# Kernel optimization log

Measured on AMD Instinct MI355X. Metric: run time of the kernel, lower is better.

The kernel has to match this reference:

```python
import jax, jax.numpy as jnp
import numpy as np


def setup_inputs() -> dict:
    key = jax.random.key(0)
    k1, k2, k3, k4 = jax.random.split(key, 4)
    N, C, H, W = 4, 256, 64, 64
    Co, kh, kw, dg = 256, 3, 3, 1
    x = jax.random.normal(k1, (N, C, H, W), dtype=jnp.float32)
    offset = jax.random.normal(k2, (N, 2 * dg * kh * kw, H, W), dtype=jnp.float32)
    mask = jax.random.uniform(k3, (N, dg * kh * kw, H, W), dtype=jnp.float32)
    weight = jax.random.normal(k4, (Co, C, kh, kw), dtype=jnp.float32) * 0.02
    bias = jnp.zeros((Co,), dtype=jnp.float32)
    return {"x": x, "offset": offset, "mask": mask, "weight": weight, "bias": bias,
            "stride": 1, "padding": 1, "dilation": 1, "deformable_groups": 1}


def _dcn_v2(x, offset, mask, weight, bias, stride, padding, dilation, dg):
    N, C, H, W = x.shape
    Co, Ci, kh, kw = weight.shape
    K = kh * kw
    Ho, Wo = offset.shape[2], offset.shape[3]
    Cg = C // dg

    off = offset.reshape(N, dg, K, 2, Ho, Wo)
    dy, dx = off[:, :, :, 0], off[:, :, :, 1]          # [N,dg,K,Ho,Wo]
    m = mask.reshape(N, dg, K, Ho, Wo)

    ki = (jnp.arange(K) // kw).astype(jnp.float32)      # kernel row index
    kj = (jnp.arange(K) % kw).astype(jnp.float32)       # kernel col index
    base_y = (jnp.arange(Ho, dtype=jnp.float32) * stride - padding)
    base_x = (jnp.arange(Wo, dtype=jnp.float32) * stride - padding)
    # sampling coordinates [N,dg,K,Ho,Wo]
    py = dy + base_y[None, None, None, :, None] + (ki * dilation)[None, None, :, None, None]
    px = dx + base_x[None, None, None, None, :] + (kj * dilation)[None, None, :, None, None]

    y0 = jnp.floor(py)
    x0 = jnp.floor(px)
    wy1 = py - y0
    wx1 = px - x0
    wy0 = 1.0 - wy1
    wx0 = 1.0 - wx1
    y0i = y0.astype(jnp.int32)
    x0i = x0.astype(jnp.int32)

    xr = x.reshape(N, dg, Cg, H * W)

    def gather(yi, xi):
        valid = ((yi >= 0) & (yi < H) & (xi >= 0) & (xi < W)).astype(x.dtype)
        idx = jnp.clip(yi, 0, H - 1) * W + jnp.clip(xi, 0, W - 1)   # [N,dg,K,Ho,Wo]
        flat = idx.reshape(N, dg, 1, K * Ho * Wo)
        g = jnp.take_along_axis(xr, flat, axis=-1).reshape(N, dg, Cg, K, Ho, Wo)
        return g * valid[:, :, None]

    sampled = (gather(y0i, x0i) * (wy0 * wx0)[:, :, None]
               + gather(y0i, x0i + 1) * (wy0 * wx1)[:, :, None]
               + gather(y0i + 1, x0i) * (wy1 * wx0)[:, :, None]
               + gather(y0i + 1, x0i + 1) * (wy1 * wx1)[:, :, None])
    sampled = sampled * m[:, :, None]                     # modulation
    sampled = sampled.reshape(N, C, K, Ho, Wo)

    out = jnp.einsum('nckhw,ock->nohw', sampled, weight.reshape(Co, C, K))
    return out + bias[None, :, None, None]


def reference(x, offset, mask, weight, bias, stride, padding, dilation, deformable_groups):
    return _dcn_v2(x, offset, mask, weight, bias, stride, padding, dilation, deformable_groups)
```

## Files before the change

kernel.cpp:

```cpp
#include <hip/hip_runtime.h>


typedef _Float16 f16x8 __attribute__((ext_vector_type(8)));
typedef _Float16 f16x4 __attribute__((ext_vector_type(4)));
typedef float f32x4 __attribute__((ext_vector_type(4)));

#define C_IN 256
#define CO   256
#define KK   9
#define HWSZ 4096
#define LDB  72
#define BUFB (64 * LDB)
#define PSTR (4 * CO * HWSZ)

struct __align__(16) SP2 { uint4 off; f16x4 w; };

static __device__ __forceinline__ f16x8 splat8(_Float16 v) {
    f16x8 r = {v, v, v, v, v, v, v, v};
    return r;
}

__global__ void transpose_x_kernel(const float* __restrict__ x,
                                   _Float16* __restrict__ xt) {
    __shared__ float tile[64][65];
    const int n  = blockIdx.z;
    const int p0 = blockIdx.x * 64;
    const int c0 = blockIdx.y * 64;
    const int tx = threadIdx.x & 63;
    const int ty = threadIdx.x >> 6;
    for (int i = 0; i < 16; ++i) {
        int c = ty * 16 + i;
        tile[c][tx] = x[((size_t)(n * C_IN + c0 + c) << 12) + p0 + tx];
    }
    __syncthreads();
    for (int i = 0; i < 16; ++i) {
        int p = ty * 16 + i;
        xt[((size_t)((n << 12) + p0 + p) << 8) + c0 + tx] = (_Float16)tile[tx][p];
    }
}

__global__ void transpose_w_kernel(const float* __restrict__ w,
                                   _Float16* __restrict__ wt2) {
    const int o = blockIdx.x;
    const int c = threadIdx.x;
    const int f = o >> 4, r = o & 15, cc = c >> 5, kq = c & 31;
    for (int kk = 0; kk < KK; ++kk) {
        int q = cc * 9 + kk;
        wt2[((f * 72 + q) * 16 + r) * 32 + kq] =
            (_Float16)w[(o * C_IN + c) * KK + kk];
    }
}

template <int NHALF>
__launch_bounds__(256, 2)
__global__ void dcn_main_kernel(const float* __restrict__ offset,
                                const float* __restrict__ mask,
                                const float* __restrict__ bias,
                                const _Float16* __restrict__ xt,
                                const _Float16* __restrict__ wt2,
                                float* __restrict__ out,
                                _Float16* __restrict__ parts) {
    constexpr int NS = 36 / NHALF;
    __shared__ SP2 sP[576];
    __shared__ _Float16 sB[2][BUFB];

    const int tid = threadIdx.x;
    const int cpx = (256 * NHALF) >> 3;
    const int lin = blockIdx.x;
    const int id  = (lin & 7) * cpx + (lin >> 3);
    const int half = (NHALF == 2) ? (id >> 8) : 0;
    const int pt   = id & 255;
    const int p0   = pt * 64;
    const int n    = p0 >> 12;
    const int phw0 = p0 & 4095;
    const int cc0  = half * 4;

    for (int t = tid; t < 576; t += 256) {
        int pl = t / 9;
        int k  = t - pl * 9;
        int phw = phw0 + pl;
        int h = phw >> 6, w = phw & 63;
        float dy = offset[(size_t)(n * 18 + 2 * k)     * HWSZ + phw];
        float dx = offset[(size_t)(n * 18 + 2 * k + 1) * HWSZ + phw];
        float mv = mask  [(size_t)(n * 9 + k)          * HWSZ + phw];
        float py = dy + (float)(h - 1 + k / 3);
        float px = dx + (float)(w - 1 + k % 3);
        float y0f = floorf(py), x0f = floorf(px);
        int y0 = (int)y0f, x0 = (int)x0f;
        float wy1 = py - y0f, wx1 = px - x0f;
        float wy0 = 1.f - wy1, wx0 = 1.f - wx1;
        int y1 = y0 + 1, x1 = x0 + 1;
        float vy0 = (y0 >= 0 && y0 < 64) ? 1.f : 0.f;
        float vy1 = (y1 >= 0 && y1 < 64) ? 1.f : 0.f;
        float vx0 = (x0 >= 0 && x0 < 64) ? 1.f : 0.f;
        float vx1 = (x1 >= 0 && x1 < 64) ? 1.f : 0.f;
        int cy0 = min(max(y0, 0), 63), cy1 = min(max(y1, 0), 63);
        int cx0 = min(max(x0, 0), 63), cx1 = min(max(x1, 0), 63);
        SP2 e;
        e.off = make_uint4((unsigned)(cy0 * 64 + cx0) << 9,
                           (unsigned)(cy0 * 64 + cx1) << 9,
                           (unsigned)(cy1 * 64 + cx0) << 9,
                           (unsigned)(cy1 * 64 + cx1) << 9);
        f16x4 wv;
        wv.x = (_Float16)(wy0 * wx0 * mv * vy0 * vx0);
        wv.y = (_Float16)(wy0 * wx1 * mv * vy0 * vx1);
        wv.z = (_Float16)(wy1 * wx0 * mv * vy1 * vx0);
        wv.w = (_Float16)(wy1 * wx1 * mv * vy1 * vx1);
        e.w = wv;
        sP[t] = e;
    }
    __syncthreads();

    const int lane = tid & 63;
    const int wid  = tid >> 6;
    const int l15  = lane & 15;
    const int lhi  = lane >> 4;

    const int pixl  = tid >> 2;
    const int oct   = tid & 3;
    const int pixl9 = pixl * 9;

    const char* xb  = (const char*)(xt + ((size_t)n << 12) * C_IN);
    const char* wtb = (const char*)wt2;

    const int vBe = l15 * LDB + lhi * 8;
    const int vWe = pixl * LDB + oct * 8;
    const unsigned chBase = (unsigned)(cc0 * 64 + oct * 16);

    unsigned voffA[4];
    for (int fm = 0; fm < 4; ++fm) {
        int fglob = wid * 4 + fm;
        voffA[fm] = (unsigned)((fglob * 72 + cc0 * 9) * 1024 + l15 * 64 + lhi * 16);
    }

    f16x8 ga[2][8];
    f16x8 aa[2][8];
    f16x4 gw[2][2];
    f32x4 acc[4][4];
    for (int i = 0; i < 4; ++i)
        for (int j = 0; j < 4; ++j)
            acc[i][j] = (f32x4){0.f, 0.f, 0.f, 0.f};

#define ISSUE_GA(T, SLOT)                                                     \
    {                                                                         \
        const SP2 e0 = sP[pixl9 + (2 * (T)) % 9];                             \
        const SP2 e1 = sP[pixl9 + (2 * (T) + 1) % 9];                         \
        gw[SLOT][0] = e0.w;                                                   \
        gw[SLOT][1] = e1.w;                                                   \
        const unsigned cE = chBase + (unsigned)(((2 * (T)) / 9) * 64);        \
        const unsigned cO = chBase + (unsigned)(((2 * (T) + 1) / 9) * 64);    \
        ga[SLOT][0] = *(const f16x8*)(xb + (e0.off.x + cE));                  \
        ga[SLOT][1] = *(const f16x8*)(xb + (e0.off.y + cE));                  \
        ga[SLOT][2] = *(const f16x8*)(xb + (e0.off.z + cE));                  \
        ga[SLOT][3] = *(const f16x8*)(xb + (e0.off.w + cE));                  \
        ga[SLOT][4] = *(const f16x8*)(xb + (e1.off.x + cO));                  \
        ga[SLOT][5] = *(const f16x8*)(xb + (e1.off.y + cO));                  \
        ga[SLOT][6] = *(const f16x8*)(xb + (e1.off.z + cO));                  \
        ga[SLOT][7] = *(const f16x8*)(xb + (e1.off.w + cO));                  \
    }

#define ISSUE_A(T, SLOT)                                                      \
    {                                                                         \
        for (int fm_ = 0; fm_ < 4; ++fm_) {                                   \
            unsigned vo_ = voffA[fm_] + (unsigned)((T) * 2048);               \
            aa[SLOT][fm_ * 2 + 0] = *(const f16x8*)(wtb + vo_);               \
            aa[SLOT][fm_ * 2 + 1] = *(const f16x8*)(wtb + vo_ + 1024);        \
        }                                                                     \
    }

#define COMBINE(SLOT, BUF)                                                    \
    {                                                                         \
        _Float16* bw_ = &sB[0][0] + (BUF) * BUFB + vWe;                       \
        f16x8 r0_ = ga[SLOT][0] * splat8(gw[SLOT][0].x)                       \
                  + ga[SLOT][1] * splat8(gw[SLOT][0].y)                       \
                  + ga[SLOT][2] * splat8(gw[SLOT][0].z)                       \
                  + ga[SLOT][3] * splat8(gw[SLOT][0].w);                      \
        f16x8 r1_ = ga[SLOT][4] * splat8(gw[SLOT][1].x)                       \
                  + ga[SLOT][5] * splat8(gw[SLOT][1].y)                       \
                  + ga[SLOT][6] * splat8(gw[SLOT][1].z)                       \
                  + ga[SLOT][7] * splat8(gw[SLOT][1].w);                      \
        *(f16x8*)(bw_)      = r0_;                                            \
        *(f16x8*)(bw_ + 32) = r1_;                                            \
    }

#define MFMA_STEP(SLOT, BUF)                                                  \
    {                                                                         \
        const _Float16* br_ = &sB[0][0] + (BUF) * BUFB + vBe;                 \
        for (int fn_ = 0; fn_ < 4; ++fn_) {                                   \
            f16x8 bE_ = *(const f16x8*)(br_ + fn_ * 16 * LDB);                \
            f16x8 bO_ = *(const f16x8*)(br_ + fn_ * 16 * LDB + 32);           \
            for (int fm_ = 0; fm_ < 4; ++fm_) {                               \
                acc[fm_][fn_] = __builtin_amdgcn_mfma_f32_16x16x32_f16(       \
                    aa[SLOT][fm_ * 2 + 0], bE_, acc[fm_][fn_], 0, 0, 0);      \
                acc[fm_][fn_] = __builtin_amdgcn_mfma_f32_16x16x32_f16(       \
                    aa[SLOT][fm_ * 2 + 1], bO_, acc[fm_][fn_], 0, 0, 0);      \
            }                                                                 \
        }                                                                     \
    }

#define BAR()                                                                 \
    {                                                                         \
        asm volatile("s_waitcnt lgkmcnt(0)" ::: "memory");                    \
        __builtin_amdgcn_s_barrier();                                         \
        asm volatile("" ::: "memory");                                        \
    }

    ISSUE_GA(0, 0)
    ISSUE_GA(1, 1)
    ISSUE_A(0, 0)
    COMBINE(0, 0)
    BAR()

#pragma unroll
    for (int s = 0; s < NS; ++s) {
        if (s + 1 < NS) ISSUE_A(s + 1, (s + 1) & 1)
        if (s + 2 < NS) ISSUE_GA(s + 2, s & 1)
        __builtin_amdgcn_sched_barrier(0);
        MFMA_STEP(s & 1, s & 1)
        if (s + 1 < NS) {
            COMBINE((s + 1) & 1, (s + 1) & 1)
            BAR()
        }
    }

    if constexpr (NHALF == 2) {
        _Float16* pp = parts + (size_t)half * PSTR;
        for (int fm = 0; fm < 4; ++fm)
            for (int fn = 0; fn < 4; ++fn) {
                int pix = phw0 + fn * 16 + l15;
                for (int r = 0; r < 4; ++r) {
                    int o = wid * 64 + fm * 16 + lhi * 4 + r;
                    pp[((size_t)(n * CO + o) << 12) + pix] =
                        (_Float16)acc[fm][fn][r];
                }
            }
    } else {
        for (int fm = 0; fm < 4; ++fm)
            for (int fn = 0; fn < 4; ++fn) {
                int pix = phw0 + fn * 16 + l15;
                for (int r = 0; r < 4; ++r) {
                    int o = wid * 64 + fm * 16 + lhi * 4 + r;
                    out[((size_t)(n * CO + o) << 12) + pix] =
                        acc[fm][fn][r] + bias[o];
                }
            }
    }
#undef ISSUE_GA
#undef ISSUE_A
#undef COMBINE
#undef MFMA_STEP
#undef BAR
}

__global__ void reduce_kernel(float* __restrict__ out,
                              const _Float16* __restrict__ parts,
                              const float* __restrict__ bias, int n8) {
    int i = blockIdx.x * blockDim.x + threadIdx.x;
    if (i >= n8) return;
    f16x8 a = ((const f16x8*)parts)[i];
    f16x8 b = ((const f16x8*)(parts + (size_t)PSTR))[i];
    float bv = bias[((i * 8) >> 12) & 255];
    f32x4 r0, r1;
    for (int e = 0; e < 4; ++e)
        r0[e] = (float)a[e] + (float)b[e] + bv;
    for (int e = 0; e < 4; ++e)
        r1[e] = (float)a[e + 4] + (float)b[e + 4] + bv;
    ((f32x4*)out)[2 * i]     = r0;
    ((f32x4*)out)[2 * i + 1] = r1;
}

extern "C" void kernel_launch(void* const* d_in, const int* in_sizes, int n_in,
                              void* d_out, int out_size, void* d_ws, size_t ws_size,
                              hipStream_t stream) {
    const float* x      = (const float*)d_in[0];
    const float* offset = (const float*)d_in[1];
    const float* mask   = (const float*)d_in[2];
    const float* weight = (const float*)d_in[3];
    const float* bias   = (const float*)d_in[4];
    float* out = (float*)d_out;

    _Float16* xt  = (_Float16*)d_ws;
    _Float16* wt2 = (_Float16*)((char*)d_ws + 8388608);
    _Float16* parts = (_Float16*)((char*)d_ws + 9568256);
    const bool split = ws_size >= (size_t)9568256 + (size_t)2 * PSTR * 2;

    transpose_x_kernel<<<dim3(64, 4, 4), 256, 0, stream>>>(x, xt);
    transpose_w_kernel<<<CO, C_IN, 0, stream>>>(weight, wt2);
    if (split) {
        dcn_main_kernel<2><<<dim3(512), 256, 0, stream>>>(offset, mask, bias,
                                                          xt, wt2, out, parts);
        reduce_kernel<<<dim3(PSTR / 8 / 256), 256, 0, stream>>>(out, parts, bias,
                                                                PSTR / 8);
    } else {
        dcn_main_kernel<1><<<dim3(256), 256, 0, stream>>>(offset, mask, bias,
                                                          xt, wt2, out, parts);
    }
}
```

Baseline: 53.67 us.

## Split deformable conv into params, explicit im2col, and GEMM kernels

Moves the per-pixel bilinear parameter computation and the deformable gather/interpolation out of the main kernel into separate params and im2col kernels that materialize an fp16 column matrix. The GEMM kernel then streams contiguous rows of this matrix instead of doing scattered gathers and combines inline, and raises the occupancy target. This removes gather latency and ALU work from the MFMA loop. In exchange it adds a large intermediate buffer write and read-back, plus two extra kernel launches.

```diff
diff --git a/kernel.cpp b/kernel.cpp
--- a/kernel.cpp
+++ b/kernel.cpp
@@ -12,6 +12,7 @@
 #define LDB  72
 #define BUFB (64 * LDB)
 #define PSTR (4 * CO * HWSZ)
+#define KROW 4608
 
 struct __align__(16) SP2 { uint4 off; f16x4 w; };
 
@@ -51,17 +52,78 @@
     }
 }
 
+__global__ void params_kernel(const float* __restrict__ offset,
+                              const float* __restrict__ mask,
+                              SP2* __restrict__ SPG) {
+    const int t = blockIdx.x * 256 + threadIdx.x;
+    const int pix = t / 9;
+    const int k   = t - pix * 9;
+    const int n   = pix >> 12;
+    const int phw = pix & 4095;
+    const int h = phw >> 6, w = phw & 63;
+    float dy = offset[(size_t)(n * 18 + 2 * k)     * HWSZ + phw];
+    float dx = offset[(size_t)(n * 18 + 2 * k + 1) * HWSZ + phw];
+    float mv = mask  [(size_t)(n * 9 + k)          * HWSZ + phw];
+    float py = dy + (float)(h - 1 + k / 3);
+    float px = dx + (float)(w - 1 + k % 3);
+    float y0f = floorf(py), x0f = floorf(px);
+    int y0 = (int)y0f, x0 = (int)x0f;
+    float wy1 = py - y0f, wx1 = px - x0f;
+    float wy0 = 1.f - wy1, wx0 = 1.f - wx1;
+    int y1 = y0 + 1, x1 = x0 + 1;
+    float vy0 = (y0 >= 0 && y0 < 64) ? 1.f : 0.f;
+    float vy1 = (y1 >= 0 && y1 < 64) ? 1.f : 0.f;
+    float vx0 = (x0 >= 0 && x0 < 64) ? 1.f : 0.f;
+    float vx1 = (x1 >= 0 && x1 < 64) ? 1.f : 0.f;
+    int cy0 = min(max(y0, 0), 63), cy1 = min(max(y1, 0), 63);
+    int cx0 = min(max(x0, 0), 63), cx1 = min(max(x1, 0), 63);
+    SP2 e;
+    e.off = make_uint4((unsigned)(cy0 * 64 + cx0) << 9,
+                       (unsigned)(cy0 * 64 + cx1) << 9,
+                       (unsigned)(cy1 * 64 + cx0) << 9,
+                       (unsigned)(cy1 * 64 + cx1) << 9);
+    f16x4 wv;
+    wv.x = (_Float16)(wy0 * wx0 * mv * vy0 * vx0);
+    wv.y = (_Float16)(wy0 * wx1 * mv * vy0 * vx1);
+    wv.z = (_Float16)(wy1 * wx0 * mv * vy1 * vx0);
+    wv.w = (_Float16)(wy1 * wx1 * mv * vy1 * vx1);
+    e.w = wv;
+    SPG[t] = e;
+}
+
+__global__ void im2col_kernel(const SP2* __restrict__ SPG,
+                              const _Float16* __restrict__ xt,
+                              _Float16* __restrict__ Bm) {
+    const int g    = blockIdx.x * 256 + threadIdx.x;
+    const int team = g >> 2;
+    const int oct  = g & 3;
+    const int pix  = team / 9;
+    const int tap  = team - pix * 9;
+    const int n    = pix >> 12;
+    const SP2 e = SPG[team];
+    const char* xb = (const char*)xt + ((size_t)n << 21);
+    char* bo = (char*)Bm + (size_t)pix * KROW + tap * 64 + oct * 16;
+#pragma unroll
+    for (int cc = 0; cc < 8; ++cc) {
+        const unsigned c_ = (unsigned)(cc * 64 + oct * 16);
+        f16x8 g0 = *(const f16x8*)(xb + (e.off.x + c_));
+        f16x8 g1 = *(const f16x8*)(xb + (e.off.y + c_));
+        f16x8 g2 = *(const f16x8*)(xb + (e.off.z + c_));
+        f16x8 g3 = *(const f16x8*)(xb + (e.off.w + c_));
+        f16x8 r = g0 * splat8(e.w.x) + g1 * splat8(e.w.y)
+                + g2 * splat8(e.w.z) + g3 * splat8(e.w.w);
+        *(f16x8*)(bo + cc * 576) = r;
+    }
+}
+
 template <int NHALF>
-__launch_bounds__(256, 2)
-__global__ void dcn_main_kernel(const float* __restrict__ offset,
-                                const float* __restrict__ mask,
+__launch_bounds__(256, 3)
+__global__ void dcn_gemm_kernel(const _Float16* __restrict__ Bm,
+                                const _Float16* __restrict__ wt2,
                                 const float* __restrict__ bias,
-                                const _Float16* __restrict__ xt,
-                                const _Float16* __restrict__ wt2,
                                 float* __restrict__ out,
                                 _Float16* __restrict__ parts) {
     constexpr int NS = 36 / NHALF;
-    __shared__ SP2 sP[576];
     __shared__ _Float16 sB[2][BUFB];
 
     const int tid = threadIdx.x;
@@ -75,57 +137,20 @@
     const int phw0 = p0 & 4095;
     const int cc0  = half * 4;
 
-    for (int t = tid; t < 576; t += 256) {
-        int pl = t / 9;
-        int k  = t - pl * 9;
-        int phw = phw0 + pl;
-        int h = phw >> 6, w = phw & 63;
-        float dy = offset[(size_t)(n * 18 + 2 * k)     * HWSZ + phw];
-        float dx = offset[(size_t)(n * 18 + 2 * k + 1) * HWSZ + phw];
-        float mv = mask  [(size_t)(n * 9 + k)          * HWSZ + phw];
-        float py = dy + (float)(h - 1 + k / 3);
-        float px = dx + (float)(w - 1 + k % 3);
-        float y0f = floorf(py), x0f = floorf(px);
-        int y0 = (int)y0f, x0 = (int)x0f;
-        float wy1 = py - y0f, wx1 = px - x0f;
-        float wy0 = 1.f - wy1, wx0 = 1.f - wx1;
-        int y1 = y0 + 1, x1 = x0 + 1;
-        float vy0 = (y0 >= 0 && y0 < 64) ? 1.f : 0.f;
-        float vy1 = (y1 >= 0 && y1 < 64) ? 1.f : 0.f;
-        float vx0 = (x0 >= 0 && x0 < 64) ? 1.f : 0.f;
-        float vx1 = (x1 >= 0 && x1 < 64) ? 1.f : 0.f;
-        int cy0 = min(max(y0, 0), 63), cy1 = min(max(y1, 0), 63);
-        int cx0 = min(max(x0, 0), 63), cx1 = min(max(x1, 0), 63);
-        SP2 e;
-        e.off = make_uint4((unsigned)(cy0 * 64 + cx0) << 9,
-                           (unsigned)(cy0 * 64 + cx1) << 9,
-                           (unsigned)(cy1 * 64 + cx0) << 9,
-                           (unsigned)(cy1 * 64 + cx1) << 9);
-        f16x4 wv;
-        wv.x = (_Float16)(wy0 * wx0 * mv * vy0 * vx0);
-        wv.y = (_Float16)(wy0 * wx1 * mv * vy0 * vx1);
-        wv.z = (_Float16)(wy1 * wx0 * mv * vy1 * vx0);
-        wv.w = (_Float16)(wy1 * wx1 * mv * vy1 * vx1);
-        e.w = wv;
-        sP[t] = e;
-    }
-    __syncthreads();
-
     const int lane = tid & 63;
     const int wid  = tid >> 6;
     const int l15  = lane & 15;
     const int lhi  = lane >> 4;
 
-    const int pixl  = tid >> 2;
-    const int oct   = tid & 3;
-    const int pixl9 = pixl * 9;
-
-    const char* xb  = (const char*)(xt + ((size_t)n << 12) * C_IN);
+    const int pixl = tid >> 2;
+    const int oct  = tid & 3;
+
     const char* wtb = (const char*)wt2;
+    const char* bmb = (const char*)Bm + (size_t)(p0) * KROW
+                    + (unsigned)(cc0 * 576);
 
     const int vBe = l15 * LDB + lhi * 8;
     const int vWe = pixl * LDB + oct * 8;
-    const unsigned chBase = (unsigned)(cc0 * 64 + oct * 16);
 
     unsigned voffA[4];
     for (int fm = 0; fm < 4; ++fm) {
@@ -133,30 +158,18 @@
         voffA[fm] = (unsigned)((fglob * 72 + cc0 * 9) * 1024 + l15 * 64 + lhi * 16);
     }
 
-    f16x8 ga[2][8];
+    f16x8 bb[2][2];
     f16x8 aa[2][8];
-    f16x4 gw[2][2];
     f32x4 acc[4][4];
     for (int i = 0; i < 4; ++i)
         for (int j = 0; j < 4; ++j)
             acc[i][j] = (f32x4){0.f, 0.f, 0.f, 0.f};
 
-#define ISSUE_GA(T, SLOT)                                                     \
-    {                                                                         \
-        const SP2 e0 = sP[pixl9 + (2 * (T)) % 9];                             \
-        const SP2 e1 = sP[pixl9 + (2 * (T) + 1) % 9];                         \
-        gw[SLOT][0] = e0.w;                                                   \
-        gw[SLOT][1] = e1.w;                                                   \
-        const unsigned cE = chBase + (unsigned)(((2 * (T)) / 9) * 64);        \
-        const unsigned cO = chBase + (unsigned)(((2 * (T) + 1) / 9) * 64);    \
-        ga[SLOT][0] = *(const f16x8*)(xb + (e0.off.x + cE));                  \
-        ga[SLOT][1] = *(const f16x8*)(xb + (e0.off.y + cE));                  \
-        ga[SLOT][2] = *(const f16x8*)(xb + (e0.off.z + cE));                  \
-        ga[SLOT][3] = *(const f16x8*)(xb + (e0.off.w + cE));                  \
-        ga[SLOT][4] = *(const f16x8*)(xb + (e1.off.x + cO));                  \
-        ga[SLOT][5] = *(const f16x8*)(xb + (e1.off.y + cO));                  \
-        ga[SLOT][6] = *(const f16x8*)(xb + (e1.off.z + cO));                  \
-        ga[SLOT][7] = *(const f16x8*)(xb + (e1.off.w + cO));                  \
+#define ISSUE_B(T, SLOT)                                                      \
+    {                                                                         \
+        const char* b_ = bmb + (size_t)pixl * KROW + (T) * 128 + oct * 16;    \
+        bb[SLOT][0] = *(const f16x8*)(b_);                                    \
+        bb[SLOT][1] = *(const f16x8*)(b_ + 64);                               \
     }
 
 #define ISSUE_A(T, SLOT)                                                      \
@@ -168,19 +181,11 @@
         }                                                                     \
     }
 
-#define COMBINE(SLOT, BUF)                                                    \
+#define BSTORE(SLOT, BUF)                                                     \
     {                                                                         \
         _Float16* bw_ = &sB[0][0] + (BUF) * BUFB + vWe;                       \
-        f16x8 r0_ = ga[SLOT][0] * splat8(gw[SLOT][0].x)                       \
-                  + ga[SLOT][1] * splat8(gw[SLOT][0].y)                       \
-                  + ga[SLOT][2] * splat8(gw[SLOT][0].z)                       \
-                  + ga[SLOT][3] * splat8(gw[SLOT][0].w);                      \
-        f16x8 r1_ = ga[SLOT][4] * splat8(gw[SLOT][1].x)                       \
-                  + ga[SLOT][5] * splat8(gw[SLOT][1].y)                       \
-                  + ga[SLOT][6] * splat8(gw[SLOT][1].z)                       \
-                  + ga[SLOT][7] * splat8(gw[SLOT][1].w);                      \
-        *(f16x8*)(bw_)      = r0_;                                            \
-        *(f16x8*)(bw_ + 32) = r1_;                                            \
+        *(f16x8*)(bw_)      = bb[SLOT][0];                                    \
+        *(f16x8*)(bw_ + 32) = bb[SLOT][1];                                    \
     }
 
 #define MFMA_STEP(SLOT, BUF)                                                  \
@@ -205,20 +210,20 @@
         asm volatile("" ::: "memory");                                        \
     }
 
-    ISSUE_GA(0, 0)
-    ISSUE_GA(1, 1)
+    ISSUE_B(0, 0)
+    ISSUE_B(1, 1)
     ISSUE_A(0, 0)
-    COMBINE(0, 0)
+    BSTORE(0, 0)
     BAR()
 
 #pragma unroll
     for (int s = 0; s < NS; ++s) {
         if (s + 1 < NS) ISSUE_A(s + 1, (s + 1) & 1)
-        if (s + 2 < NS) ISSUE_GA(s + 2, s & 1)
+        if (s + 2 < NS) ISSUE_B(s + 2, s & 1)
         __builtin_amdgcn_sched_barrier(0);
         MFMA_STEP(s & 1, s & 1)
         if (s + 1 < NS) {
-            COMBINE((s + 1) & 1, (s + 1) & 1)
+            BSTORE((s + 1) & 1, (s + 1) & 1)
             BAR()
         }
     }
@@ -245,9 +250,9 @@
                 }
             }
     }
-#undef ISSUE_GA
+#undef ISSUE_B
 #undef ISSUE_A
-#undef COMBINE
+#undef BSTORE
 #undef MFMA_STEP
 #undef BAR
 }
@@ -281,18 +286,22 @@
 
     _Float16* xt  = (_Float16*)d_ws;
     _Float16* wt2 = (_Float16*)((char*)d_ws + 8388608);
-    _Float16* parts = (_Float16*)((char*)d_ws + 9568256);
-    const bool split = ws_size >= (size_t)9568256 + (size_t)2 * PSTR * 2;
+    SP2*      SPG = (SP2*)((char*)d_ws + 9568256);
+    _Float16* Bm  = (_Float16*)((char*)d_ws + 14286848);
+    _Float16* parts = (_Float16*)((char*)d_ws + 89784320);
+    const bool split = ws_size >= (size_t)89784320 + (size_t)2 * PSTR * 2;
 
     transpose_x_kernel<<<dim3(64, 4, 4), 256, 0, stream>>>(x, xt);
     transpose_w_kernel<<<CO, C_IN, 0, stream>>>(weight, wt2);
+    params_kernel<<<dim3(576), 256, 0, stream>>>(offset, mask, SPG);
+    im2col_kernel<<<dim3(2304), 256, 0, stream>>>(SPG, xt, Bm);
     if (split) {
-        dcn_main_kernel<2><<<dim3(512), 256, 0, stream>>>(offset, mask, bias,
-                                                          xt, wt2, out, parts);
+        dcn_gemm_kernel<2><<<dim3(512), 256, 0, stream>>>(Bm, wt2, bias,
+                                                          out, parts);
         reduce_kernel<<<dim3(PSTR / 8 / 256), 256, 0, stream>>>(out, parts, bias,
                                                                 PSTR / 8);
     } else {
-        dcn_main_kernel<1><<<dim3(256), 256, 0, stream>>>(offset, mask, bias,
-                                                          xt, wt2, out, parts);
-    }
-}
+        dcn_gemm_kernel<1><<<dim3(256), 256, 0, stream>>>(Bm, wt2, bias,
+                                                          out, parts);
+    }
+}
```

Result: slower. 70.75 us (+31.8%).
